# Kernel tuning notes

Measured on AMD Instinct MI355X. Metric: run time of the kernel, lower is better.

The kernel has to match this reference:

```python
import jax, jax.numpy as jnp
import numpy as np

EPS = 1e-12
TEMPERATURE = 0.1
QUEUE_SIZE = 1024
CUTOFF_KM = 25.0
EARTH_R_KM = 6371.0088


def _normalize(x, axis=-1):
    n = jnp.linalg.norm(x, axis=axis, keepdims=True)
    return x / jnp.maximum(n, EPS)


def _haversine_km(a, b):
    # a: (B,1,2), b: (1,S,2) in degrees (lat, lon) -> (B,S) km
    ra, rb = jnp.deg2rad(a), jnp.deg2rad(b)
    dlat = rb[..., 0] - ra[..., 0]
    dlon = rb[..., 1] - ra[..., 1]
    h = jnp.sin(dlat / 2) ** 2 + jnp.cos(ra[..., 0]) * jnp.cos(rb[..., 0]) * jnp.sin(dlon / 2) ** 2
    return 2.0 * EARTH_R_KM * jnp.arcsin(jnp.sqrt(jnp.clip(h, 0.0, 1.0)))


def setup_inputs() -> dict:
    key = jax.random.key(0)
    k1, k2, k3, k4, k5 = jax.random.split(key, 5)
    A, B, F, S = 3, 256, 512, 100000
    V = jax.random.normal(k1, (A, B, F), dtype=jnp.float32)
    L = jax.random.normal(k2, (B, F), dtype=jnp.float32)
    # gps as (lat, lon) degrees
    gps = jax.random.uniform(k3, (B, 2), dtype=jnp.float32) * jnp.array([120.0, 360.0]) - jnp.array([60.0, 180.0])
    support_feats = jax.random.normal(k4, (S, F), dtype=jnp.float32)
    support_gps = jax.random.uniform(k5, (S, 2), dtype=jnp.float32) * jnp.array([120.0, 360.0]) - jnp.array([60.0, 180.0])
    return {"V": V, "L": L, "gps": gps, "support_feats": support_feats, "support_gps": support_gps}


def reference(V, L, gps, support_feats, support_gps):
    T, Q = TEMPERATURE, QUEUE_SIZE
    L_norm = _normalize(L, axis=1)                      # (B,F)
    org = _normalize(V[0] * L_norm, axis=1)             # (B,F)
    aug = _normalize(V[1:] * L_norm, axis=2)            # (A-1,B,F)

    # nearest_neighbours (no_grad): per-batch NN in support set by dot-product sim
    sims = jnp.einsum('sf,bf->sb', support_feats, org)  # (S,B)
    nn_idx = jnp.argmax(sims, axis=0)                   # (B,)
    nn = _normalize(support_feats[nn_idx], axis=1)      # (B,F)
    nn = jax.lax.stop_gradient(nn)

    pos = jnp.exp(jnp.einsum('abf,bf->ab', aug, nn) / T)  # (A-1,B)
    batch_den = jnp.sum(pos, axis=0)                       # (B,)

    # nn_negative_queue (no_grad): first Q support rows farther than 25 km, zeros if fewer
    dist = _haversine_km(gps[:, None, :], support_gps[None, :, :])  # (B,S)
    far = dist > CUTOFF_KM                                          # (B,S)
    order = jnp.argsort(jnp.logical_not(far), axis=1)[:, :Q]        # stable: far rows first, in order
    valid = jnp.take_along_axis(far, order, axis=1)                 # (B,Q)
    negq = jnp.where(valid[..., None], support_feats[order], 0.0)   # (B,Q,F)
    negq = jax.lax.stop_gradient(_normalize(negq, axis=2))          # zero rows stay zero

    queue_den = jnp.sum(jnp.exp(jnp.einsum('bqf,bf->bq', negq, nn) / T), axis=1)  # (B,)

    loss = jnp.mean(-batch_den / (batch_den + queue_den))
    return loss
```

## Files before the change

kernel.cpp:

```cpp
#include <hip/hip_runtime.h>
#include <hip/hip_bf16.h>
#include <math.h>

#define B_N 256
#define F_N 512
#define S_N 100000
#define Q_N 1024
#define EPSF 1e-12f
#define BM 128
#define NBLK ((S_N + BM - 1) / BM)
#define CAND_MAX 64
#define MARGIN 0.125f
#define RS_SPLIT 16

typedef __attribute__((ext_vector_type(8))) short short8v;
typedef __attribute__((ext_vector_type(4))) float f32x4;

__device__ __forceinline__ unsigned short f2bf(float x) {
  unsigned u = __float_as_uint(x);
  u = u + 0x7FFFu + ((u >> 16) & 1u);
  return (unsigned short)(u >> 16);
}

__device__ __forceinline__ float warpReduceSum(float v) {
  #pragma unroll
  for (int o = 32; o > 0; o >>= 1) v += __shfl_down(v, o);
  return v;
}

__device__ __forceinline__ float blockReduceSum256(float v, float* buf) {
  v = warpReduceSum(v);
  int lane = threadIdx.x & 63, w = threadIdx.x >> 6;
  __syncthreads();
  if (lane == 0) buf[w] = v;
  __syncthreads();
  return buf[0] + buf[1] + buf[2] + buf[3];
}

__device__ __forceinline__ void async_copy16(void* lds, const void* g) {
  __builtin_amdgcn_global_load_lds(
      (const __attribute__((address_space(1))) unsigned int*)g,
      (__attribute__((address_space(3))) unsigned int*)lds, 16, 0, 0);
}

__device__ __forceinline__ void cvt8hi(const float4 a, const float4 b,
                                       short8v& hi) {
  union { unsigned u[4]; short8v v; } H;
  union { __hip_bfloat162 b2; unsigned u; } c;
  c.b2 = __float22bfloat162_rn(make_float2(a.x, a.y)); H.u[0] = c.u;
  c.b2 = __float22bfloat162_rn(make_float2(a.z, a.w)); H.u[1] = c.u;
  c.b2 = __float22bfloat162_rn(make_float2(b.x, b.y)); H.u[2] = c.u;
  c.b2 = __float22bfloat162_rn(make_float2(b.z, b.w)); H.u[3] = c.u;
  hi = H.v;
}

__global__ __launch_bounds__(256) void k_prep(const float* __restrict__ V,
    const float* __restrict__ L, unsigned short* __restrict__ orghi,
    float* __restrict__ org, float* __restrict__ aug) {
  __shared__ float buf[4];
  int b = blockIdx.x, t = threadIdx.x;
  const float2 lv = *(const float2*)&L[b * F_N + t * 2];
  float ss = blockReduceSum256(lv.x * lv.x + lv.y * lv.y, buf);
  float invL = 1.0f / fmaxf(sqrtf(ss), EPSF);
  float lnx = lv.x * invL, lny = lv.y * invL;
  #pragma unroll
  for (int a = 0; a < 3; ++a) {
    const float2 vv = *(const float2*)&V[(a * B_N + b) * F_N + t * 2];
    float yx = vv.x * lnx, yy = vv.y * lny;
    float s2 = blockReduceSum256(yx * yx + yy * yy, buf);
    float inv = 1.0f / fmaxf(sqrtf(s2), EPSF);
    if (a == 0) {
      float ox = yx * inv, oy = yy * inv;
      int f = t * 2;
      int kt = f >> 5, kk = f & 31, sub = kk >> 3, pos = kk & 7;
      int off = kt * 8192 + b * 32 + sub * 8 + pos;
      ushort2 hv; hv.x = f2bf(ox); hv.y = f2bf(oy);
      *(ushort2*)&orghi[off] = hv;
      float2 of; of.x = ox; of.y = oy;
      *(float2*)&org[b * F_N + f] = of;
    } else {
      float* dst = &aug[((a - 1) * B_N + b) * F_N + t * 2];
      dst[0] = yx * inv;
      dst[1] = yy * inv;
    }
  }
}

__global__ __launch_bounds__(256, 2) void k_sims(const float* __restrict__ support,
    const unsigned short* __restrict__ orghi, float* __restrict__ blkmax) {
  __shared__ __align__(16) unsigned char smem[65536];

  int t = threadIdx.x;
  int lane = t & 63, w = t >> 6;
  int r15 = lane & 15, ks = lane >> 4;
  int s0 = blockIdx.x * BM;

  f32x4 acc0[16], acc1[16];
  #pragma unroll
  for (int n = 0; n < 16; ++n) {
    acc0[n] = (f32x4){0.f, 0.f, 0.f, 0.f};
    acc1[n] = (f32x4){0.f, 0.f, 0.f, 0.f};
  }

  int row0 = s0 + w * 32 + r15;
  int row1 = row0 + 16;
  if (row0 > S_N - 1) row0 = S_N - 1;
  if (row1 > S_N - 1) row1 = S_N - 1;
  const float* ap0 = support + (size_t)row0 * F_N + ks * 8;
  const float* ap1 = support + (size_t)row1 * F_N + ks * 8;

  const unsigned char* bsrc = (const unsigned char*)orghi + t * 16;

  {
    unsigned char* dst = smem + t * 16;
    #pragma unroll
    for (int p = 0; p < 8; ++p) async_copy16(dst + p * 4096, bsrc + p * 4096);
  }
  __builtin_amdgcn_sched_barrier(0);
  float4 a00a = *(const float4*)(ap0);
  float4 a00b = *(const float4*)(ap0 + 4);
  float4 a01a = *(const float4*)(ap0 + 32);
  float4 a01b = *(const float4*)(ap0 + 36);
  float4 a10a = *(const float4*)(ap1);
  float4 a10b = *(const float4*)(ap1 + 4);
  float4 a11a = *(const float4*)(ap1 + 32);
  float4 a11b = *(const float4*)(ap1 + 36);
  __builtin_amdgcn_sched_barrier(0);
  asm volatile("s_waitcnt vmcnt(8)" ::: "memory");
  __builtin_amdgcn_s_barrier();
  __builtin_amdgcn_sched_barrier(0);

  const int rbase = r15 * 64 + ks * 16;

  #pragma unroll 1
  for (int it = 0; it < 8; ++it) {
    unsigned char* bbuf = smem + (it & 1) * 32768;
    short8v f00, f01, f10, f11;
    cvt8hi(a00a, a00b, f00);
    cvt8hi(a01a, a01b, f01);
    cvt8hi(a10a, a10b, f10);
    cvt8hi(a11a, a11b, f11);
    if (it < 7) {
      const unsigned char* src = bsrc + (it + 1) * 32768;
      unsigned char* dst = smem + ((it + 1) & 1) * 32768 + t * 16;
      #pragma unroll
      for (int p = 0; p < 8; ++p) async_copy16(dst + p * 4096, src + p * 4096);
      __builtin_amdgcn_sched_barrier(0);
      a00a = *(const float4*)(ap0 + (it + 1) * 64);
      a00b = *(const float4*)(ap0 + (it + 1) * 64 + 4);
      a01a = *(const float4*)(ap0 + (it + 1) * 64 + 32);
      a01b = *(const float4*)(ap0 + (it + 1) * 64 + 36);
      a10a = *(const float4*)(ap1 + (it + 1) * 64);
      a10b = *(const float4*)(ap1 + (it + 1) * 64 + 4);
      a11a = *(const float4*)(ap1 + (it + 1) * 64 + 32);
      a11b = *(const float4*)(ap1 + (it + 1) * 64 + 36);
      __builtin_amdgcn_sched_barrier(0);
    }
    const unsigned char* bp = bbuf + rbase;
    __builtin_amdgcn_s_setprio(1);
    #pragma unroll
    for (int n = 0; n < 16; ++n) {
      short8v bh0 = *(const short8v*)(bp + n * 1024);
      short8v bh1 = *(const short8v*)(bp + 16384 + n * 1024);
      acc0[n] = __builtin_amdgcn_mfma_f32_16x16x32_bf16(f00, bh0, acc0[n], 0, 0, 0);
      acc1[n] = __builtin_amdgcn_mfma_f32_16x16x32_bf16(f10, bh0, acc1[n], 0, 0, 0);
      acc0[n] = __builtin_amdgcn_mfma_f32_16x16x32_bf16(f01, bh1, acc0[n], 0, 0, 0);
      acc1[n] = __builtin_amdgcn_mfma_f32_16x16x32_bf16(f11, bh1, acc1[n], 0, 0, 0);
    }
    __builtin_amdgcn_s_setprio(0);
    __builtin_amdgcn_sched_barrier(0);
    if (it < 7) {
      asm volatile("s_waitcnt vmcnt(8)" ::: "memory");
      __builtin_amdgcn_s_barrier();
    } else {
      __syncthreads();
    }
    __builtin_amdgcn_sched_barrier(0);
  }

  float* wkf = (float*)smem;
  #pragma unroll
  for (int n = 0; n < 16; ++n) {
    float bv = -INFINITY;
    #pragma unroll
    for (int r = 0; r < 4; ++r) {
      bv = fmaxf(bv, acc0[n][r]);
      bv = fmaxf(bv, acc1[n][r]);
    }
    bv = fmaxf(bv, __shfl_xor(bv, 16));
    bv = fmaxf(bv, __shfl_xor(bv, 32));
    if (lane < 16) wkf[w * 256 + n * 16 + lane] = bv;
  }
  __syncthreads();
  {
    float m4 = fmaxf(fmaxf(wkf[t], wkf[256 + t]),
                     fmaxf(wkf[512 + t], wkf[768 + t]));
    blkmax[(size_t)t * NBLK + blockIdx.x] = m4;
  }
}

__global__ __launch_bounds__(256) void k_cand(const float* __restrict__ blkmax,
    int* __restrict__ cand, int* __restrict__ cnt) {
  __shared__ float redf[4];
  __shared__ int lcand[CAND_MAX];
  __shared__ int lcnt;
  int b = blockIdx.x, t = threadIdx.x;
  int lane = t & 63, w = t >> 6;
  if (t == 0) lcnt = 0;

  const float* bm = blkmax + (size_t)b * NBLK;
  float mx = -INFINITY;
  for (int rb = t; rb < NBLK; rb += 256) mx = fmaxf(mx, bm[rb]);
  #pragma unroll
  for (int o = 32; o > 0; o >>= 1) mx = fmaxf(mx, __shfl_xor(mx, o));
  __syncthreads();
  if (lane == 0) redf[w] = mx;
  __syncthreads();
  mx = fmaxf(fmaxf(redf[0], redf[1]), fmaxf(redf[2], redf[3]));
  float thr = mx - MARGIN;

  for (int rb = t; rb < NBLK; rb += 256) {
    if (bm[rb] >= thr) {
      int sl = atomicAdd(&lcnt, 1);
      if (sl < CAND_MAX) lcand[sl] = rb;
    }
  }
  __syncthreads();
  int nc = lcnt < CAND_MAX ? lcnt : CAND_MAX;
  if (t < CAND_MAX) cand[b * CAND_MAX + t] = (t < nc) ? lcand[t] : 0;
  if (t == 0) cnt[b] = nc;
}

__global__ __launch_bounds__(256) void k_rescore(const float* __restrict__ support,
    const float* __restrict__ org, const int* __restrict__ cand,
    const int* __restrict__ cnt, double* __restrict__ rval,
    int* __restrict__ ridx) {
  __shared__ float orgs[F_N];
  __shared__ double rv[4];
  __shared__ int ri[4];
  int b = blockIdx.x >> 4, jj = blockIdx.x & (RS_SPLIT - 1);
  int t = threadIdx.x;
  int lane = t & 63, w = t >> 6;

  orgs[t] = org[b * F_N + t];
  orgs[256 + t] = org[b * F_N + 256 + t];
  __syncthreads();

  int nc = cnt[b];
  double bv = -1e300;
  int bi = 0x7FFFFFFF;
  for (int sl = (jj >> 1); sl < nc; sl += RS_SPLIT / 2) {
    int blk = cand[b * CAND_MAX + sl];
    int rbase = blk * BM + (jj & 1) * 64 + w * 16;
    for (int rr = 0; rr < 16; ++rr) {
      int s = rbase + rr;
      if (s >= S_N) continue;
      const float4* rp = (const float4*)(support + (size_t)s * F_N) + lane * 2;
      float4 r0 = rp[0], r1 = rp[1];
      const float4 n0 = *(const float4*)&orgs[lane * 8];
      const float4 n1 = *(const float4*)&orgs[lane * 8 + 4];
      double d = (double)r0.x * (double)n0.x + (double)r0.y * (double)n0.y +
                 (double)r0.z * (double)n0.z + (double)r0.w * (double)n0.w +
                 (double)r1.x * (double)n1.x + (double)r1.y * (double)n1.y +
                 (double)r1.z * (double)n1.z + (double)r1.w * (double)n1.w;
      #pragma unroll
      for (int o = 32; o > 0; o >>= 1) d += __shfl_xor(d, o);
      if (d > bv || (d == bv && s < bi)) { bv = d; bi = s; }
    }
  }
  if (lane == 0) { rv[w] = bv; ri[w] = bi; }
  __syncthreads();
  if (t == 0) {
    double fv = rv[0]; int fi = ri[0];
    #pragma unroll
    for (int i = 1; i < 4; ++i)
      if (rv[i] > fv || (rv[i] == fv && ri[i] < fi)) { fv = rv[i]; fi = ri[i]; }
    rval[b * RS_SPLIT + jj] = fv;
    ridx[b * RS_SPLIT + jj] = fi;
  }
}

__global__ __launch_bounds__(256) void k_nn(const float* __restrict__ support,
    const double* __restrict__ rval, const int* __restrict__ ridx,
    const float* __restrict__ aug, float* __restrict__ nn,
    float* __restrict__ bden) {
  __shared__ float buf[4];
  __shared__ int sidx;
  int b = blockIdx.x, t = threadIdx.x;
  if (t < 64) {
    double v = (t < RS_SPLIT) ? rval[b * RS_SPLIT + t] : -1e300;
    int i = (t < RS_SPLIT) ? ridx[b * RS_SPLIT + t] : 0x7FFFFFFF;
    #pragma unroll
    for (int o = 32; o > 0; o >>= 1) {
      double ov = __shfl_xor(v, o);
      int oi = __shfl_xor(i, o);
      if (ov > v || (ov == v && oi < i)) { v = ov; i = oi; }
    }
    if (t == 0) sidx = i;
  }
  __syncthreads();
  int idx = sidx;
  const float2 rvv = *(const float2*)&support[(size_t)idx * F_N + t * 2];
  float ss = blockReduceSum256(rvv.x * rvv.x + rvv.y * rvv.y, buf);
  float inv = 1.0f / fmaxf(sqrtf(ss), EPSF);
  float nx = rvv.x * inv, ny = rvv.y * inv;
  nn[b * F_N + t * 2] = nx;
  nn[b * F_N + t * 2 + 1] = ny;
  const float2 a0 = *(const float2*)&aug[(0 * B_N + b) * F_N + t * 2];
  const float2 a1 = *(const float2*)&aug[(1 * B_N + b) * F_N + t * 2];
  float d0 = blockReduceSum256(a0.x * nx + a0.y * ny, buf);
  float d1 = blockReduceSum256(a1.x * nx + a1.y * ny, buf);
  if (t == 0) bden[b] = expf(d0 * 10.0f) + expf(d1 * 10.0f);
}

__global__ __launch_bounds__(256) void k_qdot(const float* __restrict__ support,
    const float* __restrict__ gps, const float* __restrict__ sgps,
    const float* __restrict__ nn, double* __restrict__ qpart) {
  __shared__ float nns[F_N];
  __shared__ int qi[256];
  __shared__ int wtot[4];
  __shared__ double wacc[4];
  int b = blockIdx.x >> 2, c = blockIdx.x & 3;
  int t = threadIdx.x;
  int lane = t & 63, w = t >> 6;

  *(float2*)&nns[t * 2] = *(const float2*)&nn[b * F_N + t * 2];

  const float DEG2RAD = 0.017453292519943295f;
  float la = gps[b * 2] * DEG2RAD;
  float lo = gps[b * 2 + 1] * DEG2RAD;
  float ca = cosf(la);
  double xd = 25.0 / (2.0 * 6371.0088);
  float hcut = (float)(sin(xd) * sin(xd));

  int cnt = 0;
  int qlo = c * 256;
  for (int base = 0; base < S_N; base += 256) {
    int s = base + t;
    bool far = false;
    if (s < S_N) {
      float lb = sgps[s * 2] * DEG2RAD;
      float ob = sgps[s * 2 + 1] * DEG2RAD;
      float sl = sinf((lb - la) * 0.5f);
      float so = sinf((ob - lo) * 0.5f);
      float h = sl * sl + ca * cosf(lb) * so * so;
      far = h > hcut;
    }
    unsigned long long m = __ballot(far);
    if (lane == 0) wtot[w] = (int)__popcll(m);
    __syncthreads();
    int offs = cnt;
    for (int wi = 0; wi < w; ++wi) offs += wtot[wi];
    if (far) {
      int pos = offs + (int)__popcll(m & ((1ull << lane) - 1ull));
      int rel = pos - qlo;
      if (rel >= 0 && rel < 256) qi[rel] = s;
    }
    cnt += wtot[0] + wtot[1] + wtot[2] + wtot[3];
    __syncthreads();
    if (cnt >= Q_N) break;
  }
  int nvalid = cnt < Q_N ? cnt : Q_N;
  __syncthreads();

  double acc = 0.0;
  for (int j = 0; j < 64; ++j) {
    int q = qlo + w * 64 + j;
    if (q >= nvalid) break;
    int row = qi[w * 64 + j];
    const float4* rp = (const float4*)&support[(size_t)row * F_N + lane * 8];
    float4 r0 = rp[0], r1 = rp[1];
    const float4 n0 = *(const float4*)&nns[lane * 8];
    const float4 n1 = *(const float4*)&nns[lane * 8 + 4];
    float dot = r0.x * n0.x + r0.y * n0.y + r0.z * n0.z + r0.w * n0.w +
                r1.x * n1.x + r1.y * n1.y + r1.z * n1.z + r1.w * n1.w;
    float ssq = r0.x * r0.x + r0.y * r0.y + r0.z * r0.z + r0.w * r0.w +
                r1.x * r1.x + r1.y * r1.y + r1.z * r1.z + r1.w * r1.w;
    #pragma unroll
    for (int o = 32; o > 0; o >>= 1) {
      dot += __shfl_xor(dot, o);
      ssq += __shfl_xor(ssq, o);
    }
    float val = dot / fmaxf(sqrtf(ssq), EPSF);
    acc += (double)expf(val * 10.0f);
  }
  if (lane == 0) wacc[w] = acc;
  __syncthreads();
  if (t == 0) {
    int got = nvalid - qlo;
    if (got < 0) got = 0; if (got > 256) got = 256;
    int inval = 256 - got;
    qpart[blockIdx.x] = wacc[0] + wacc[1] + wacc[2] + wacc[3] + (double)inval;
  }
}

__global__ __launch_bounds__(256) void k_final(const double* __restrict__ qpart,
    const float* __restrict__ bden, float* __restrict__ out) {
  __shared__ double buf[4];
  int t = threadIdx.x;
  double qd = qpart[t * 4] + qpart[t * 4 + 1] + qpart[t * 4 + 2] + qpart[t * 4 + 3];
  double bd = (double)bden[t];
  double v = -bd / (bd + qd);
  #pragma unroll
  for (int o = 32; o > 0; o >>= 1) v += __shfl_down(v, o);
  if ((t & 63) == 0) buf[t >> 6] = v;
  __syncthreads();
  if (t == 0) out[0] = (float)((buf[0] + buf[1] + buf[2] + buf[3]) / 256.0);
}

extern "C" void kernel_launch(void* const* d_in, const int* in_sizes, int n_in,
                              void* d_out, int out_size, void* d_ws, size_t ws_size,
                              hipStream_t stream) {
  const float* V = (const float*)d_in[0];
  const float* L = (const float*)d_in[1];
  const float* gps = (const float*)d_in[2];
  const float* support = (const float*)d_in[3];
  const float* sgps = (const float*)d_in[4];
  float* out = (float*)d_out;

  char* ws = (char*)d_ws;
  float* bden = (float*)(ws + 2048);
  double* qpart = (double*)(ws + 4096);
  int* cnt = (int*)(ws + 12288);
  int* cand = (int*)(ws + 16384);
  double* rval = (double*)(ws + 81920);
  int* ridx = (int*)(ws + 114688);
  unsigned short* orghi = (unsigned short*)(ws + 131072);
  float* org = (float*)(ws + 131072 + 262144);
  float* aug = (float*)(ws + 131072 + 262144 + 524288);
  float* nn = (float*)(ws + 131072 + 262144 + 524288 + 1048576);
  float* blkmax = (float*)(ws + 131072 + 262144 + 524288 + 1048576 + 524288);

  k_prep<<<256, 256, 0, stream>>>(V, L, orghi, org, aug);
  k_sims<<<NBLK, 256, 0, stream>>>(support, orghi, blkmax);
  k_cand<<<256, 256, 0, stream>>>(blkmax, cand, cnt);
  k_rescore<<<256 * RS_SPLIT, 256, 0, stream>>>(support, org, cand, cnt, rval, ridx);
  k_nn<<<256, 256, 0, stream>>>(support, rval, ridx, aug, nn, bden);
  k_qdot<<<1024, 256, 0, stream>>>(support, gps, sgps, nn, qpart);
  k_final<<<1, 256, 0, stream>>>(qpart, bden, out);
}
```

Measured before the change: 167.2 us.

## Fold candidate selection into sims via atomic max and deepen sims pipeline

Result: slower. 212.9 us (+27.4%).

```diff
diff --git a/kernel.cpp b/kernel.cpp
--- a/kernel.cpp
+++ b/kernel.cpp
@@ -9,7 +9,6 @@
 #define EPSF 1e-12f
 #define BM 128
 #define NBLK ((S_N + BM - 1) / BM)
-#define CAND_MAX 64
 #define MARGIN 0.125f
 #define RS_SPLIT 16
 
@@ -20,6 +19,14 @@
   unsigned u = __float_as_uint(x);
   u = u + 0x7FFFu + ((u >> 16) & 1u);
   return (unsigned short)(u >> 16);
+}
+__device__ __forceinline__ unsigned mapf(float x) {
+  unsigned u = __float_as_uint(x);
+  return (u & 0x80000000u) ? ~u : (u | 0x80000000u);
+}
+__device__ __forceinline__ float unmapf(unsigned m) {
+  unsigned u = (m & 0x80000000u) ? (m & 0x7FFFFFFFu) : ~m;
+  return __uint_as_float(u);
 }
 
 __device__ __forceinline__ float warpReduceSum(float v) {
@@ -56,9 +63,11 @@
 
 __global__ __launch_bounds__(256) void k_prep(const float* __restrict__ V,
     const float* __restrict__ L, unsigned short* __restrict__ orghi,
-    float* __restrict__ org, float* __restrict__ aug) {
+    float* __restrict__ org, float* __restrict__ aug,
+    unsigned* __restrict__ gmax) {
   __shared__ float buf[4];
   int b = blockIdx.x, t = threadIdx.x;
+  if (t == 0) gmax[b] = 0u;
   const float2 lv = *(const float2*)&L[b * F_N + t * 2];
   float ss = blockReduceSum256(lv.x * lv.x + lv.y * lv.y, buf);
   float invL = 1.0f / fmaxf(sqrtf(ss), EPSF);
@@ -87,7 +96,8 @@
 }
 
 __global__ __launch_bounds__(256, 2) void k_sims(const float* __restrict__ support,
-    const unsigned short* __restrict__ orghi, float* __restrict__ blkmax) {
+    const unsigned short* __restrict__ orghi, float* __restrict__ blkmax,
+    unsigned* __restrict__ gmax) {
   __shared__ __align__(16) unsigned char smem[65536];
 
   int t = threadIdx.x;
@@ -110,73 +120,75 @@
   const float* ap1 = support + (size_t)row1 * F_N + ks * 8;
 
   const unsigned char* bsrc = (const unsigned char*)orghi + t * 16;
+  const int rbase = r15 * 64 + ks * 16;
+
+  float4 a0a, a0b, a1a, a1b;
 
   {
     unsigned char* dst = smem + t * 16;
     #pragma unroll
-    for (int p = 0; p < 8; ++p) async_copy16(dst + p * 4096, bsrc + p * 4096);
+    for (int p = 0; p < 4; ++p) async_copy16(dst + p * 4096, bsrc + p * 4096);
   }
   __builtin_amdgcn_sched_barrier(0);
-  float4 a00a = *(const float4*)(ap0);
-  float4 a00b = *(const float4*)(ap0 + 4);
-  float4 a01a = *(const float4*)(ap0 + 32);
-  float4 a01b = *(const float4*)(ap0 + 36);
-  float4 a10a = *(const float4*)(ap1);
-  float4 a10b = *(const float4*)(ap1 + 4);
-  float4 a11a = *(const float4*)(ap1 + 32);
-  float4 a11b = *(const float4*)(ap1 + 36);
+  a0a = *(const float4*)(ap0);
+  a0b = *(const float4*)(ap0 + 4);
+  a1a = *(const float4*)(ap1);
+  a1b = *(const float4*)(ap1 + 4);
   __builtin_amdgcn_sched_barrier(0);
-  asm volatile("s_waitcnt vmcnt(8)" ::: "memory");
-  __builtin_amdgcn_s_barrier();
-  __builtin_amdgcn_sched_barrier(0);
-
-  const int rbase = r15 * 64 + ks * 16;
-
-  #pragma unroll 1
-  for (int it = 0; it < 8; ++it) {
-    unsigned char* bbuf = smem + (it & 1) * 32768;
-    short8v f00, f01, f10, f11;
-    cvt8hi(a00a, a00b, f00);
-    cvt8hi(a01a, a01b, f01);
-    cvt8hi(a10a, a10b, f10);
-    cvt8hi(a11a, a11b, f11);
-    if (it < 7) {
-      const unsigned char* src = bsrc + (it + 1) * 32768;
-      unsigned char* dst = smem + ((it + 1) & 1) * 32768 + t * 16;
-      #pragma unroll
-      for (int p = 0; p < 8; ++p) async_copy16(dst + p * 4096, src + p * 4096);
-      __builtin_amdgcn_sched_barrier(0);
-      a00a = *(const float4*)(ap0 + (it + 1) * 64);
-      a00b = *(const float4*)(ap0 + (it + 1) * 64 + 4);
-      a01a = *(const float4*)(ap0 + (it + 1) * 64 + 32);
-      a01b = *(const float4*)(ap0 + (it + 1) * 64 + 36);
-      a10a = *(const float4*)(ap1 + (it + 1) * 64);
-      a10b = *(const float4*)(ap1 + (it + 1) * 64 + 4);
-      a11a = *(const float4*)(ap1 + (it + 1) * 64 + 32);
-      a11b = *(const float4*)(ap1 + (it + 1) * 64 + 36);
-      __builtin_amdgcn_sched_barrier(0);
-    }
-    const unsigned char* bp = bbuf + rbase;
-    __builtin_amdgcn_s_setprio(1);
-    #pragma unroll
-    for (int n = 0; n < 16; ++n) {
-      short8v bh0 = *(const short8v*)(bp + n * 1024);
-      short8v bh1 = *(const short8v*)(bp + 16384 + n * 1024);
-      acc0[n] = __builtin_amdgcn_mfma_f32_16x16x32_bf16(f00, bh0, acc0[n], 0, 0, 0);
-      acc1[n] = __builtin_amdgcn_mfma_f32_16x16x32_bf16(f10, bh0, acc1[n], 0, 0, 0);
-      acc0[n] = __builtin_amdgcn_mfma_f32_16x16x32_bf16(f01, bh1, acc0[n], 0, 0, 0);
-      acc1[n] = __builtin_amdgcn_mfma_f32_16x16x32_bf16(f11, bh1, acc1[n], 0, 0, 0);
-    }
-    __builtin_amdgcn_s_setprio(0);
+  #pragma unroll
+  for (int s = 1; s <= 2; ++s) {
+    const unsigned char* src = bsrc + s * 16384;
+    unsigned char* dst = smem + s * 16384 + t * 16;
+    #pragma unroll
+    for (int p = 0; p < 4; ++p) async_copy16(dst + p * 4096, src + p * 4096);
     __builtin_amdgcn_sched_barrier(0);
-    if (it < 7) {
-      asm volatile("s_waitcnt vmcnt(8)" ::: "memory");
-      __builtin_amdgcn_s_barrier();
-    } else {
-      __syncthreads();
-    }
-    __builtin_amdgcn_sched_barrier(0);
-  }
+  }
+
+  #define WAITV(n) asm volatile("s_waitcnt vmcnt(" #n ")" ::: "memory")
+  #define ITERK(K, WN)                                                         \
+    do {                                                                        \
+      WAITV(WN);                                      \
+      __builtin_amdgcn_s_barrier();                                             \
+      __builtin_amdgcn_sched_barrier(0);                                        \
+      short8v f0, f1;                                                           \
+      cvt8hi(a0a, a0b, f0);    \
+      cvt8hi(a1a, a1b, f1);                                                     \
+      __builtin_amdgcn_sched_barrier(0);                                        \
+      if ((K) < 15) {             \
+        a0a = *(const float4*)(ap0 + ((K) + 1) * 32);                           \
+        a0b = *(const float4*)(ap0 + ((K) + 1) * 32 + 4);                       \
+        a1a = *(const float4*)(ap1 + ((K) + 1) * 32);                           \
+        a1b = *(const float4*)(ap1 + ((K) + 1) * 32 + 4);                       \
+        __builtin_amdgcn_sched_barrier(0);                                      \
+      }                                                                         \
+      if ((K) < 13) {                          \
+        const unsigned char* src_ = bsrc + ((K) + 3) * 16384;                   \
+        unsigned char* dst_ = smem + (((K) + 3) & 3) * 16384 + t * 16;          \
+        _Pragma("unroll")                                                       \
+        for (int p = 0; p < 4; ++p)                                             \
+          async_copy16(dst_ + p * 4096, src_ + p * 4096);                       \
+        __builtin_amdgcn_sched_barrier(0);                                      \
+      }                                                                         \
+      const unsigned char* bp_ = smem + ((K) & 3) * 16384 + rbase;              \
+      __builtin_amdgcn_s_setprio(1);                                            \
+      _Pragma("unroll")                                                         \
+      for (int n = 0; n < 16; ++n) {                                            \
+        short8v bh = *(const short8v*)(bp_ + n * 1024);                         \
+        acc0[n] = __builtin_amdgcn_mfma_f32_16x16x32_bf16(f0, bh, acc0[n], 0, 0, 0); \
+        acc1[n] = __builtin_amdgcn_mfma_f32_16x16x32_bf16(f1, bh, acc1[n], 0, 0, 0); \
+      }                                                                         \
+      __builtin_amdgcn_s_setprio(0);                                            \
+      __builtin_amdgcn_sched_barrier(0);                                        \
+    } while (0)
+
+  ITERK(0, 12);  ITERK(1, 12);  ITERK(2, 12);  ITERK(3, 12);
+  ITERK(4, 12);  ITERK(5, 12);  ITERK(6, 12);  ITERK(7, 12);
+  ITERK(8, 12);  ITERK(9, 12);  ITERK(10, 12); ITERK(11, 12);
+  ITERK(12, 12); ITERK(13, 12); ITERK(14, 8);  ITERK(15, 4);
+  #undef ITERK
+  #undef WAITV
+
+  __syncthreads();
 
   float* wkf = (float*)smem;
   #pragma unroll
@@ -196,44 +208,13 @@
     float m4 = fmaxf(fmaxf(wkf[t], wkf[256 + t]),
                      fmaxf(wkf[512 + t], wkf[768 + t]));
     blkmax[(size_t)t * NBLK + blockIdx.x] = m4;
-  }
-}
-
-__global__ __launch_bounds__(256) void k_cand(const float* __restrict__ blkmax,
-    int* __restrict__ cand, int* __restrict__ cnt) {
-  __shared__ float redf[4];
-  __shared__ int lcand[CAND_MAX];
-  __shared__ int lcnt;
-  int b = blockIdx.x, t = threadIdx.x;
-  int lane = t & 63, w = t >> 6;
-  if (t == 0) lcnt = 0;
-
-  const float* bm = blkmax + (size_t)b * NBLK;
-  float mx = -INFINITY;
-  for (int rb = t; rb < NBLK; rb += 256) mx = fmaxf(mx, bm[rb]);
-  #pragma unroll
-  for (int o = 32; o > 0; o >>= 1) mx = fmaxf(mx, __shfl_xor(mx, o));
-  __syncthreads();
-  if (lane == 0) redf[w] = mx;
-  __syncthreads();
-  mx = fmaxf(fmaxf(redf[0], redf[1]), fmaxf(redf[2], redf[3]));
-  float thr = mx - MARGIN;
-
-  for (int rb = t; rb < NBLK; rb += 256) {
-    if (bm[rb] >= thr) {
-      int sl = atomicAdd(&lcnt, 1);
-      if (sl < CAND_MAX) lcand[sl] = rb;
-    }
-  }
-  __syncthreads();
-  int nc = lcnt < CAND_MAX ? lcnt : CAND_MAX;
-  if (t < CAND_MAX) cand[b * CAND_MAX + t] = (t < nc) ? lcand[t] : 0;
-  if (t == 0) cnt[b] = nc;
+    atomicMax(&gmax[t], mapf(m4));
+  }
 }
 
 __global__ __launch_bounds__(256) void k_rescore(const float* __restrict__ support,
-    const float* __restrict__ org, const int* __restrict__ cand,
-    const int* __restrict__ cnt, double* __restrict__ rval,
+    const float* __restrict__ org, const float* __restrict__ blkmax,
+    const unsigned* __restrict__ gmax, double* __restrict__ rval,
     int* __restrict__ ridx) {
   __shared__ float orgs[F_N];
   __shared__ double rv[4];
@@ -246,15 +227,17 @@
   orgs[256 + t] = org[b * F_N + 256 + t];
   __syncthreads();
 
-  int nc = cnt[b];
+  float thr = unmapf(gmax[b]) - MARGIN;
+  const float* bm = blkmax + (size_t)b * NBLK;
+
   double bv = -1e300;
   int bi = 0x7FFFFFFF;
-  for (int sl = (jj >> 1); sl < nc; sl += RS_SPLIT / 2) {
-    int blk = cand[b * CAND_MAX + sl];
-    int rbase = blk * BM + (jj & 1) * 64 + w * 16;
-    for (int rr = 0; rr < 16; ++rr) {
-      int s = rbase + rr;
-      if (s >= S_N) continue;
+  for (int rb = jj; rb < NBLK; rb += RS_SPLIT) {
+    if (bm[rb] < thr) continue;
+    int rbase = rb * BM + w * 32;
+    for (int j = 0; j < 32; ++j) {
+      int s = rbase + j;
+      if (s >= S_N) break;
       const float4* rp = (const float4*)(support + (size_t)s * F_N) + lane * 2;
       float4 r0 = rp[0], r1 = rp[1];
       const float4 n0 = *(const float4*)&orgs[lane * 8];
@@ -421,8 +404,7 @@
   char* ws = (char*)d_ws;
   float* bden = (float*)(ws + 2048);
   double* qpart = (double*)(ws + 4096);
-  int* cnt = (int*)(ws + 12288);
-  int* cand = (int*)(ws + 16384);
+  unsigned* gmax = (unsigned*)(ws + 12288);
   double* rval = (double*)(ws + 81920);
   int* ridx = (int*)(ws + 114688);
   unsigned short* orghi = (unsigned short*)(ws + 131072);
@@ -431,10 +413,9 @@
   float* nn = (float*)(ws + 131072 + 262144 + 524288 + 1048576);
   float* blkmax = (float*)(ws + 131072 + 262144 + 524288 + 1048576 + 524288);
 
-  k_prep<<<256, 256, 0, stream>>>(V, L, orghi, org, aug);
-  k_sims<<<NBLK, 256, 0, stream>>>(support, orghi, blkmax);
-  k_cand<<<256, 256, 0, stream>>>(blkmax, cand, cnt);
-  k_rescore<<<256 * RS_SPLIT, 256, 0, stream>>>(support, org, cand, cnt, rval, ridx);
+  k_prep<<<256, 256, 0, stream>>>(V, L, orghi, org, aug, gmax);
+  k_sims<<<NBLK, 256, 0, stream>>>(support, orghi, blkmax, gmax);
+  k_rescore<<<256 * RS_SPLIT, 256, 0, stream>>>(support, org, blkmax, gmax, rval, ridx);
   k_nn<<<256, 256, 0, stream>>>(support, rval, ridx, aug, nn, bden);
   k_qdot<<<1024, 256, 0, stream>>>(support, gps, sgps, nn, qpart);
   k_final<<<1, 256, 0, stream>>>(qpart, bden, out);
```
